# Kernel tuning notes

Measured on AMD Instinct MI355X. Metric: run time of the kernel, lower is better.

Reference implementation:

```python
import jax, jax.numpy as jnp
import numpy as np

H = 2048      # hidden_dim
DI = 4096     # intermediate_size
N = 128       # state_size
NH = 64       # num_heads
P = 64        # head_dim
K = 4         # conv kernel
CH = 256      # chunk size
L = 4096      # seq len
DT_MIN, DT_MAX = 1e-3, 1e2


def setup_inputs() -> dict:
    key = jax.random.key(0)
    ks = jax.random.split(key, 8)
    conv_dim = DI + 2 * N
    x = jax.random.normal(ks[0], (L, H), jnp.float32)
    W_in = jax.random.normal(ks[1], (DI + 2 * N + NH, H), jnp.float32) / np.sqrt(H)
    conv_w = jax.random.normal(ks[2], (conv_dim, 1, K), jnp.float32) / np.sqrt(K)
    conv_b = jax.random.normal(ks[3], (conv_dim,), jnp.float32) * 0.01
    u = jax.random.uniform(ks[4], (NH,))
    dt = jnp.exp(u * (np.log(0.1) - np.log(0.001)) + np.log(0.001))
    dt = jnp.maximum(dt, 1e-4)
    dt_bias = dt + jnp.log(-jnp.expm1(-dt))   # inverse-softplus init
    A_log = jnp.log(jax.random.uniform(ks[5], (NH,), minval=1.0, maxval=16.0))
    D = jnp.ones((NH,), jnp.float32)
    norm_w = jnp.ones((DI,), jnp.float32)
    W_out = jax.random.normal(ks[6], (H, DI), jnp.float32) / np.sqrt(DI)
    return dict(x=x, W_in=W_in, conv_w=conv_w, conv_b=conv_b, dt_bias=dt_bias,
                A_log=A_log, D=D, norm_w=norm_w, W_out=W_out)


def _causal_decay(a):
    # a: [..., T] per-step log-decays -> exp(segment sum) as lower-tri [..., T, T]
    T = a.shape[-1]
    strict = jnp.tril(jnp.ones((T, T), bool), -1)
    full = jnp.tril(jnp.ones((T, T), bool), 0)
    s = jnp.cumsum(jnp.where(strict, a[..., None], 0.0), axis=-2)
    return jnp.where(full, jnp.exp(s), 0.0)


def reference(x, W_in, conv_w, conv_b, dt_bias, A_log, D, norm_w, W_out):
    conv_dim = DI + 2 * N
    xBCdt = x @ W_in.T                                  # [L, DI+2N+NH]
    xBC, dt = xBCdt[:, :conv_dim], xBCdt[:, conv_dim:]
    # causal depthwise conv1d + SiLU
    z = jax.lax.conv_general_dilated(
        xBC.T[None], conv_w, (1,), [(K - 1, 0)],
        dimension_numbers=('NCH', 'OIH', 'NCH'),
        feature_group_count=conv_dim)[0] + conv_b[:, None]
    xBC = jax.nn.silu(z.T)                              # [L, conv_dim]
    x_ssm = xBC[:, :DI].reshape(L, NH, P)
    Bm = xBC[:, DI:DI + N]                              # [L, N] shared over heads
    Cm = xBC[:, DI + N:]                                # [L, N]
    dt = jnp.clip(jax.nn.softplus(dt + dt_bias), DT_MIN, DT_MAX)  # [L, NH]
    A = -jnp.exp(A_log.astype(jnp.float32))             # [NH]
    dA = dt * A                                         # [L, NH]
    xdt = x_ssm * dt[:, :, None]                        # [L, NH, P]
    nc = L // CH
    xc = xdt.reshape(nc, CH, NH, P)
    Bc = Bm.reshape(nc, CH, N)
    Cc = Cm.reshape(nc, CH, N)
    dAc = dA.reshape(nc, CH, NH)
    A_cs = jnp.cumsum(dAc, axis=1)                      # [c, k, h]
    # intra-chunk (diagonal blocks)
    Lmat = _causal_decay(dAc.transpose(0, 2, 1))        # [c, h, k, k]
    Y_diag = jnp.einsum('ckn,csn,chks,cshp->ckhp', Cc, Bc, Lmat, xc)
    # per-chunk right states
    decay_states = jnp.exp(A_cs[:, -1:, :] - A_cs)      # [c, k, h]
    states = jnp.einsum('ckn,ckh,ckhp->chpn', Bc, decay_states, xc)
    # inter-chunk recurrence (no initial state)
    chunk_sum = A_cs[:, -1, :].T                        # [h, c]
    dec = _causal_decay(jnp.pad(chunk_sum, ((0, 0), (1, 0))))  # [h, c+1, c+1]
    states = jnp.concatenate([jnp.zeros((1, NH, P, N), states.dtype), states], 0)
    new_states = jnp.einsum('hzc,chpn->zhpn', dec, states)      # [c+1, h, p, n]
    prev = new_states[:-1]                              # [c, h, p, n]
    Y_off = jnp.einsum('ckn,chpn,ckh->ckhp', Cc, prev, jnp.exp(A_cs))
    Y = (Y_diag + Y_off).reshape(L, NH, P) + x_ssm * D[None, :, None]
    y = Y.reshape(L, DI)
    # RMSNorm
    var = jnp.mean(jnp.square(y.astype(jnp.float32)), -1, keepdims=True)
    y = (y * jax.lax.rsqrt(var + 1e-6)) * norm_w
    return y @ W_out.T
```

## Files before the change

### kernel.cpp

```cpp
#include <hip/hip_runtime.h>


typedef __bf16 bf16;
typedef __bf16 bf16x8 __attribute__((ext_vector_type(8)));
typedef __bf16 bf16x4 __attribute__((ext_vector_type(4)));
typedef float  f32x4  __attribute__((ext_vector_type(4)));

#define DEV static __device__ __forceinline__

DEV f32x4 mfma16(bf16x8 a, bf16x8 b, f32x4 c) {
  return __builtin_amdgcn_mfma_f32_16x16x32_bf16(a, b, c, 0, 0, 0);
}

DEV void gll16(const bf16* g, bf16* l) {
  __builtin_amdgcn_global_load_lds(
      (const __attribute__((address_space(1))) unsigned int*)g,
      (__attribute__((address_space(3))) unsigned int*)l, 16, 0, 0);
}

#define BAR()   asm volatile("s_barrier" ::: "memory")
#define VMW(n)  asm volatile("s_waitcnt vmcnt(" #n ")" ::: "memory")

template <int NT, int LD, bool F32OUT>
__global__ __launch_bounds__(512, 4) void gemm_kernel(
    const bf16* __restrict__ Abase, const bf16* __restrict__ Bbase,
    float* __restrict__ Cf, bf16* __restrict__ Cb0, bf16* __restrict__ Cb1,
    int ldc, int ntN) {
  __shared__ __align__(16) bf16 lds[3 * 12288];
  const int tid = threadIdx.x;
  const int wid = tid >> 6, lane = tid & 63;
  const int lrow = lane & 15;
  const int lc = lane >> 4;
  const int wm = wid & 3, wn = wid >> 2;
  const int bx = blockIdx.x / ntN, by = blockIdx.x % ntN;
  const int row0 = bx * 256, col0 = by * 128;
  const bf16* A = Abase + (size_t)blockIdx.y * (NT * 32);
  const bf16* B = Bbase + (size_t)blockIdx.y * (NT * 32);

  const bf16* gA[2];
  const bf16* gB0;
#pragma unroll
  for (int q = 0; q < 2; ++q) {
    int P = q * 8192 + tid * 16;
    int Lq = P ^ (((P >> 7) & 3) << 4);
    int srow = Lq >> 6;
    int selem = (Lq & 63) >> 1;
    gA[q] = A + (size_t)(row0 + srow) * LD + selem;
  }
  {
    int P = tid * 16;
    int Lq = P ^ (((P >> 7) & 3) << 4);
    int srow = Lq >> 6;
    int selem = (Lq & 63) >> 1;
    gB0 = B + (size_t)(col0 + srow) * LD + selem;
  }
  auto stage = [&](int s, int ko) {
    bf16* sl = lds + s * 12288;
    gll16(gA[0] + ko, sl + tid * 8);
    gll16(gA[1] + ko, sl + 4096 + tid * 8);
    gll16(gB0 + ko, sl + 8192 + tid * 8);
  };
  auto rdA = [&](int s, int m) -> bf16x8 {
    int row = wm * 64 + m * 16 + lrow;
    int off = row * 64 + ((lc ^ ((row >> 1) & 3)) << 4);
    return *(const bf16x8*)((const char*)lds + s * 24576 + off);
  };
  auto rdB = [&](int s, int n) -> bf16x8 {
    int row = wn * 64 + n * 16 + lrow;
    int off = row * 64 + ((lc ^ ((row >> 1) & 3)) << 4);
    return *(const bf16x8*)((const char*)lds + s * 24576 + 16384 + off);
  };

  f32x4 acc[4][4] = {};
  stage(0, 0);
  stage(1, 32);
  int rs = 0, ws = 2;
  for (int t = 0; t < NT; ++t) {
    if (t + 1 < NT) { VMW(3); } else { VMW(0); }
    BAR();
    if (t + 2 < NT) stage(ws, (t + 2) * 32);
    bf16x8 b0 = rdB(rs, 0), b1 = rdB(rs, 1), b2 = rdB(rs, 2), b3 = rdB(rs, 3);
#pragma unroll
    for (int m = 0; m < 4; ++m) {
      bf16x8 a = rdA(rs, m);
      acc[m][0] = mfma16(a, b0, acc[m][0]);
      acc[m][1] = mfma16(a, b1, acc[m][1]);
      acc[m][2] = mfma16(a, b2, acc[m][2]);
      acc[m][3] = mfma16(a, b3, acc[m][3]);
    }
    rs = (rs == 2) ? 0 : rs + 1;
    ws = (ws == 2) ? 0 : ws + 1;
  }
  const int orow = lc * 4;
  if (F32OUT) {
#pragma unroll
    for (int m = 0; m < 4; ++m)
#pragma unroll
      for (int n = 0; n < 4; ++n)
#pragma unroll
        for (int i = 0; i < 4; ++i) {
          int r = row0 + wm * 64 + m * 16 + orow + i;
          int c = col0 + wn * 64 + n * 16 + lrow;
          Cf[(size_t)r * ldc + c] = acc[m][n][i];
        }
  } else {
    bf16* C = blockIdx.y ? Cb1 : Cb0;
#pragma unroll
    for (int m = 0; m < 4; ++m)
#pragma unroll
      for (int n = 0; n < 4; ++n)
#pragma unroll
        for (int i = 0; i < 4; ++i) {
          int r = row0 + wm * 64 + m * 16 + orow + i;
          int c = col0 + wn * 64 + n * 16 + lrow;
          C[(size_t)r * ldc + c] = (bf16)acc[m][n][i];
        }
  }
}

__global__ __launch_bounds__(256) void add2b_kernel(
    const bf16* __restrict__ a, const bf16* __restrict__ b,
    float* __restrict__ o, long n8) {
  long i = (long)blockIdx.x * blockDim.x + threadIdx.x;
  long stride = (long)gridDim.x * blockDim.x;
  for (; i < n8; i += stride) {
    bf16x8 va = ((const bf16x8*)a)[i];
    bf16x8 vb = ((const bf16x8*)b)[i];
    float4 o0, o1;
    o0.x = (float)va[0] + (float)vb[0];
    o0.y = (float)va[1] + (float)vb[1];
    o0.z = (float)va[2] + (float)vb[2];
    o0.w = (float)va[3] + (float)vb[3];
    o1.x = (float)va[4] + (float)vb[4];
    o1.y = (float)va[5] + (float)vb[5];
    o1.z = (float)va[6] + (float)vb[6];
    o1.w = (float)va[7] + (float)vb[7];
    ((float4*)o)[i * 2] = o0;
    ((float4*)o)[i * 2 + 1] = o1;
  }
}

__global__ __launch_bounds__(256) void cast_f2b_kernel(
    const float* __restrict__ in, bf16* __restrict__ out, long n4) {
  long i = (long)blockIdx.x * blockDim.x + threadIdx.x;
  long stride = (long)gridDim.x * blockDim.x;
  for (; i < n4; i += stride) {
    float4 v = ((const float4*)in)[i];
    bf16x4 o = {(bf16)v.x, (bf16)v.y, (bf16)v.z, (bf16)v.w};
    ((bf16x4*)out)[i] = o;
  }
}

__global__ __launch_bounds__(256) void cast_pad_kernel(
    const float* __restrict__ in, bf16* __restrict__ out, long n4, long valid4) {
  long i = (long)blockIdx.x * blockDim.x + threadIdx.x;
  long stride = (long)gridDim.x * blockDim.x;
  for (; i < n4; i += stride) {
    bf16x4 o = {(bf16)0.f, (bf16)0.f, (bf16)0.f, (bf16)0.f};
    if (i < valid4) {
      float4 v = ((const float4*)in)[i];
      o = bf16x4{(bf16)v.x, (bf16)v.y, (bf16)v.z, (bf16)v.w};
    }
    ((bf16x4*)out)[i] = o;
  }
}

__global__ __launch_bounds__(256) void dt_scan_kernel(
    const float* __restrict__ xBCdt, const float* __restrict__ dt_bias,
    const float* __restrict__ A_log, float* __restrict__ dt,
    float* __restrict__ Acs, float* __restrict__ decayO,
    float* __restrict__ expAcs, float* __restrict__ csum) {
  const int c = blockIdx.x, h = blockIdx.y;
  const int k = threadIdx.x;
  const int t = c * 256 + k;
  __shared__ float buf[256];
  float raw = xBCdt[(size_t)t * 4608 + 4352 + h] + dt_bias[h];
  float dtv = raw > 20.f ? raw : log1pf(__expf(raw));
  dtv = fminf(fmaxf(dtv, 0.001f), 100.f);
  dt[(size_t)t * 64 + h] = dtv;
  float dA = -__expf(A_log[h]) * dtv;
  buf[k] = dA;
  __syncthreads();
  for (int off = 1; off < 256; off <<= 1) {
    float add = (k >= off) ? buf[k - off] : 0.f;
    __syncthreads();
    buf[k] += add;
    __syncthreads();
  }
  float v = buf[k];
  float total = buf[255];
  size_t base = (size_t)(c * 64 + h) * 256 + k;
  Acs[base] = v;
  expAcs[base] = __expf(v);
  decayO[base] = __expf(total - v);
  if (k == 0) csum[c * 64 + h] = total;
}

__global__ __launch_bounds__(256) void conv_kernel(
    const float* __restrict__ xBCdt, const float* __restrict__ conv_w,
    const float* __restrict__ conv_b, const float* __restrict__ dt,
    bf16* __restrict__ XS, bf16* __restrict__ XDT_T, bf16* __restrict__ Bm,
    bf16* __restrict__ BT, bf16* __restrict__ Cm) {
  const int t0 = blockIdx.x * 64;
  const int c0 = blockIdx.y * 64;
  __shared__ float lin[67 * 64];
  __shared__ bf16 tr[64 * 72];
  const int tid = threadIdx.x;
  for (int idx = tid; idx < 67 * 64; idx += 256) {
    int r = idx >> 6, cc = idx & 63;
    int gt = t0 + r - 3;
    lin[idx] = (gt >= 0) ? xBCdt[(size_t)gt * 4608 + c0 + cc] : 0.f;
  }
  __syncthreads();
  const int cl = tid & 63, tg = tid >> 6;
  const int ch = c0 + cl;
  const float w0 = conv_w[ch * 4 + 0], w1 = conv_w[ch * 4 + 1];
  const float w2 = conv_w[ch * 4 + 2], w3 = conv_w[ch * 4 + 3];
  const float bb = conv_b[ch];
  float vals[16];
  for (int j = 0; j < 16; ++j) {
    int tl = tg * 16 + j;
    float s = bb + lin[tl * 64 + cl] * w0 + lin[(tl + 1) * 64 + cl] * w1 +
              lin[(tl + 2) * 64 + cl] * w2 + lin[(tl + 3) * 64 + cl] * w3;
    vals[j] = s / (1.f + __expf(-s));
  }
  if (c0 < 4096) {
    const int hh = c0 >> 6;
    for (int j = 0; j < 16; ++j) {
      int t = t0 + tg * 16 + j;
      XS[(size_t)t * 4096 + ch] = (bf16)vals[j];
    }
    __syncthreads();
    for (int j = 0; j < 16; ++j) {
      int tl = tg * 16 + j;
      float dtv = dt[(size_t)(t0 + tl) * 64 + hh];
      tr[cl * 72 + tl] = (bf16)(vals[j] * dtv);
    }
    __syncthreads();
    int p = tid >> 2, toff = (tid & 3) * 16;
    bf16* dst = XDT_T + (size_t)(hh * 64 + p) * 4096 + t0 + toff;
    *(bf16x8*)(dst) = *(const bf16x8*)(tr + p * 72 + toff);
    *(bf16x8*)(dst + 8) = *(const bf16x8*)(tr + p * 72 + toff + 8);
  } else if (c0 < 4224) {
    const int n0 = c0 - 4096;
    for (int j = 0; j < 16; ++j) {
      int t = t0 + tg * 16 + j;
      Bm[(size_t)t * 128 + n0 + cl] = (bf16)vals[j];
    }
    __syncthreads();
    for (int j = 0; j < 16; ++j) tr[cl * 72 + tg * 16 + j] = (bf16)vals[j];
    __syncthreads();
    int p = tid >> 2, toff = (tid & 3) * 16;
    bf16* dst = BT + (size_t)(n0 + p) * 4096 + t0 + toff;
    *(bf16x8*)(dst) = *(const bf16x8*)(tr + p * 72 + toff);
    *(bf16x8*)(dst + 8) = *(const bf16x8*)(tr + p * 72 + toff + 8);
  } else {
    const int n0 = c0 - 4224;
    for (int j = 0; j < 16; ++j) {
      int t = t0 + tg * 16 + j;
      Cm[(size_t)t * 128 + n0 + cl] = (bf16)vals[j];
    }
  }
}

__global__ __launch_bounds__(256) void gmat_kernel(
    const bf16* __restrict__ Cm, const bf16* __restrict__ Bm,
    bf16* __restrict__ G) {
  const int c = blockIdx.x, kt = blockIdx.y, st = blockIdx.z;
  const int tid = threadIdx.x;
  const int wave = tid >> 6, lane = tid & 63;
  const int lrow = lane & 15, lk = (lane >> 4) * 8;
  const int wr = (wave >> 1) * 64, wc = (wave & 1) * 64;
  f32x4 acc[4][4] = {};
  for (int kk = 0; kk < 4; ++kk) {
    bf16x8 aF[4], bF[4];
    for (int m = 0; m < 4; ++m)
      aF[m] = *(const bf16x8*)(Cm + (size_t)(c * 256 + kt * 128 + wr + m * 16 + lrow) * 128 + kk * 32 + lk);
    for (int n = 0; n < 4; ++n)
      bF[n] = *(const bf16x8*)(Bm + (size_t)(c * 256 + st * 128 + wc + n * 16 + lrow) * 128 + kk * 32 + lk);
    for (int m = 0; m < 4; ++m)
      for (int n = 0; n < 4; ++n)
        acc[m][n] = mfma16(aF[m], bF[n], acc[m][n]);
  }
  const int orow = (lane >> 4) * 4;
  for (int m = 0; m < 4; ++m)
    for (int n = 0; n < 4; ++n)
      for (int i = 0; i < 4; ++i) {
        int k = kt * 128 + wr + m * 16 + orow + i;
        int s = st * 128 + wc + n * 16 + lrow;
        G[((size_t)c * 256 + k) * 256 + s] = (bf16)acc[m][n][i];
      }
}

__global__ __launch_bounds__(256) void states_kernel(
    const bf16* __restrict__ XDT_T, const bf16* __restrict__ BT,
    const float* __restrict__ decayO, float* __restrict__ states) {
  const int c = blockIdx.x, h = blockIdx.y;
  __shared__ bf16 Ap[64 * 264];
  __shared__ float sDec[256];
  const int tid = threadIdx.x;
  const int wave = tid >> 6, lane = tid & 63;
  const int lrow = lane & 15, lk = (lane >> 4) * 8;
  sDec[tid] = decayO[(size_t)(c * 64 + h) * 256 + tid];
  __syncthreads();
  {
    int p = tid >> 2, kb = (tid & 3) * 64;
    const bf16* src = XDT_T + (size_t)(h * 64 + p) * 4096 + c * 256 + kb;
    for (int j = 0; j < 8; ++j) {
      bf16x8 v = *(const bf16x8*)(src + j * 8);
      bf16x8 o;
      for (int i = 0; i < 8; ++i) o[i] = (bf16)((float)v[i] * sDec[kb + j * 8 + i]);
      *(bf16x8*)(Ap + p * 264 + kb + j * 8) = o;
    }
  }
  __syncthreads();
  const int nb = wave * 32;
  f32x4 acc[4][2] = {};
  for (int kk = 0; kk < 8; ++kk) {
    bf16x8 aF[4], bF[2];
    for (int m = 0; m < 4; ++m)
      aF[m] = *(const bf16x8*)(Ap + (m * 16 + lrow) * 264 + kk * 32 + lk);
    for (int n = 0; n < 2; ++n)
      bF[n] = *(const bf16x8*)(BT + (size_t)(nb + n * 16 + lrow) * 4096 + c * 256 + kk * 32 + lk);
    for (int m = 0; m < 4; ++m)
      for (int n = 0; n < 2; ++n)
        acc[m][n] = mfma16(aF[m], bF[n], acc[m][n]);
  }
  float* st = states + (size_t)(c * 64 + h) * 64 * 128;
  const int orow = (lane >> 4) * 4;
  for (int m = 0; m < 4; ++m)
    for (int n = 0; n < 2; ++n)
      for (int i = 0; i < 4; ++i)
        st[(size_t)(m * 16 + orow + i) * 128 + nb + n * 16 + lrow] = acc[m][n][i];
}

__global__ __launch_bounds__(128) void chunk_rec_kernel(
    const float* __restrict__ states, const float* __restrict__ csum,
    bf16* __restrict__ prev) {
  const int h = blockIdx.x, p = blockIdx.y;
  const int n = threadIdx.x;
  size_t base = (size_t)h * 64 * 128 + (size_t)p * 128 + n;
  float run = 0.f;
  for (int c = 0; c < 16; ++c) {
    size_t idx = (size_t)c * 64 * 64 * 128 + base;
    prev[idx] = (bf16)run;
    run = run * __expf(csum[c * 64 + h]) + states[idx];
  }
}

__global__ __launch_bounds__(256) void ydiag_kernel(
    const bf16* __restrict__ Cm, const bf16* __restrict__ prev,
    const bf16* __restrict__ Gb, const float* __restrict__ Acs,
    const float* __restrict__ expAcs, const bf16* __restrict__ XDT_T,
    float* __restrict__ Y) {
  const int c = blockIdx.x, h = blockIdx.y;
  __shared__ float sAcs[256];
  __shared__ float sExp[256];
  __shared__ __align__(16) bf16 pv[64 * 136];
  __shared__ __align__(16) bf16 xd[64 * 264];
  const int tid = threadIdx.x;
  const int wave = tid >> 6, lane = tid & 63;
  const int lrow = lane & 15, lk = (lane >> 4) * 8;
  const int wv16 = wave * 16;
  sAcs[tid] = Acs[(size_t)(c * 64 + h) * 256 + tid];
  sExp[tid] = expAcs[(size_t)(c * 64 + h) * 256 + tid];
  {
    int r = tid >> 2, q = (tid & 3) * 32;
    const bf16* src = prev + (size_t)(c * 64 + h) * 8192 + r * 128 + q;
    bf16* dst = pv + r * 136 + q;
    for (int j = 0; j < 4; ++j)
      *(bf16x8*)(dst + j * 8) = *(const bf16x8*)(src + j * 8);
  }
  {
    int r = tid >> 2, q = (tid & 3) * 64;
    const bf16* src = XDT_T + (size_t)(h * 64 + r) * 4096 + c * 256 + q;
    bf16* dst = xd + r * 264 + q;
    for (int j = 0; j < 8; ++j)
      *(bf16x8*)(dst + j * 8) = *(const bf16x8*)(src + j * 8);
  }
  __syncthreads();
  f32x4 acc[4][4] = {};
  bf16x8 aYo[4][4];
#pragma unroll
  for (int kk = 0; kk < 4; ++kk)
#pragma unroll
    for (int m = 0; m < 4; ++m)
      aYo[kk][m] = *(const bf16x8*)(Cm + (size_t)(c * 256 + m * 64 + wv16 + lrow) * 128 + kk * 32 + lk);
#pragma unroll
  for (int kk = 0; kk < 4; ++kk) {
    bf16x8 bF[4];
#pragma unroll
    for (int n = 0; n < 4; ++n)
      bF[n] = *(const bf16x8*)(pv + (n * 16 + lrow) * 136 + kk * 32 + lk);
#pragma unroll
    for (int m = 0; m < 4; ++m)
#pragma unroll
      for (int n = 0; n < 4; ++n)
        acc[m][n] = mfma16(aYo[kk][m], bF[n], acc[m][n]);
  }
  const int orow = (lane >> 4) * 4;
#pragma unroll
  for (int m = 0; m < 4; ++m)
#pragma unroll
    for (int i = 0; i < 4; ++i) {
      float e = sExp[m * 64 + wv16 + orow + i];
      for (int n = 0; n < 4; ++n) acc[m][n][i] *= e;
    }
  const bf16* Gp = Gb + (size_t)c * 65536;
#pragma unroll
  for (int stile = 0; stile < 4; ++stile) {
    const int s0 = stile * 64;
    bf16x8 graw[2][4];
#pragma unroll
    for (int kk = 0; kk < 2; ++kk)
#pragma unroll
      for (int m = 0; m < 4; ++m)
        if (m * 64 + wv16 + 15 >= s0) {
          int row = m * 64 + wv16 + lrow;
          graw[kk][m] = *(const bf16x8*)(Gp + (size_t)row * 256 + s0 + kk * 32 + lk);
        }
    bf16x8 bF[2][4];
#pragma unroll
    for (int kk = 0; kk < 2; ++kk)
#pragma unroll
      for (int n = 0; n < 4; ++n)
        bF[kk][n] = *(const bf16x8*)(xd + (n * 16 + lrow) * 264 + s0 + kk * 32 + lk);
#pragma unroll
    for (int kk = 0; kk < 2; ++kk)
#pragma unroll
      for (int m = 0; m < 4; ++m) {
        if (m * 64 + wv16 + 15 < s0) continue;
        const int row = m * 64 + wv16 + lrow;
        const float ak = sAcs[row];
        bf16x8 af;
#pragma unroll
        for (int j = 0; j < 8; ++j) {
          int s = s0 + kk * 32 + lk + j;
          float v = (float)graw[kk][m][j] * __expf(ak - sAcs[s]);
          if (s > row) v = 0.f;
          af[j] = (bf16)v;
        }
#pragma unroll
        for (int n = 0; n < 4; ++n)
          acc[m][n] = mfma16(af, bF[kk][n], acc[m][n]);
      }
  }
#pragma unroll
  for (int m = 0; m < 4; ++m)
#pragma unroll
    for (int n = 0; n < 4; ++n)
#pragma unroll
      for (int i = 0; i < 4; ++i) {
        int t = c * 256 + m * 64 + wv16 + orow + i;
        int col = h * 64 + n * 16 + lrow;
        Y[(size_t)t * 4096 + col] = acc[m][n][i];
      }
}

__global__ __launch_bounds__(256) void rmsnorm_kernel(
    const float* __restrict__ Y, const bf16* __restrict__ XS,
    const float* __restrict__ Dp, const float* __restrict__ norm_w,
    bf16* __restrict__ out) {
  const int row = blockIdx.x;
  const float4* y4 = (const float4*)(Y + (size_t)row * 4096);
  const bf16x4* xs4 = (const bf16x4*)(XS + (size_t)row * 4096);
  float4 v[4];
  float ss = 0.f;
  for (int j = 0; j < 4; ++j) {
    int c4 = threadIdx.x + j * 256;
    float4 y = y4[c4];
    bf16x4 xs = xs4[c4];
    float d = Dp[(c4 * 4) >> 6];
    y.x += (float)xs[0] * d;
    y.y += (float)xs[1] * d;
    y.z += (float)xs[2] * d;
    y.w += (float)xs[3] * d;
    v[j] = y;
    ss += y.x * y.x + y.y * y.y + y.z * y.z + y.w * y.w;
  }
  for (int off = 32; off; off >>= 1) ss += __shfl_down(ss, off, 64);
  __shared__ float ws[4];
  if ((threadIdx.x & 63) == 0) ws[threadIdx.x >> 6] = ss;
  __syncthreads();
  float scale = rsqrtf((ws[0] + ws[1] + ws[2] + ws[3]) / 4096.f + 1e-6f);
  for (int j = 0; j < 4; ++j) {
    int col = (threadIdx.x + j * 256) * 4;
    float4 w = *(const float4*)(norm_w + col);
    bf16x4 o = {(bf16)(v[j].x * scale * w.x), (bf16)(v[j].y * scale * w.y),
                (bf16)(v[j].z * scale * w.z), (bf16)(v[j].w * scale * w.w)};
    *(bf16x4*)(out + (size_t)row * 4096 + col) = o;
  }
}

extern "C" void kernel_launch(void* const* d_in, const int* in_sizes, int n_in,
                              void* d_out, int out_size, void* d_ws, size_t ws_size,
                              hipStream_t stream) {
  const float* x       = (const float*)d_in[0];
  const float* W_in    = (const float*)d_in[1];
  const float* conv_w  = (const float*)d_in[2];
  const float* conv_b  = (const float*)d_in[3];
  const float* dt_bias = (const float*)d_in[4];
  const float* A_log   = (const float*)d_in[5];
  const float* Dp      = (const float*)d_in[6];
  const float* norm_w  = (const float*)d_in[7];
  const float* W_out   = (const float*)d_in[8];

  size_t o = 0;
  char* base = (char*)d_ws;
  auto take = [&](size_t b) {
    char* p = base + o;
    o += (b + 255) & ~(size_t)255;
    return (void*)p;
  };
  bf16*  xb     = (bf16*)take((size_t)4096 * 2048 * 2);
  bf16*  winb   = (bf16*)take((size_t)4608 * 2048 * 2);
  float* xBCdt  = (float*)take((size_t)4096 * 4608 * 4);
  float* dtg    = (float*)take((size_t)4096 * 64 * 4);
  float* Acs    = (float*)take((size_t)4096 * 64 * 4);
  float* decayO = (float*)take((size_t)4096 * 64 * 4);
  float* expA   = (float*)take((size_t)4096 * 64 * 4);
  float* csum   = (float*)take((size_t)16 * 64 * 4);
  bf16*  XS     = (bf16*)take((size_t)4096 * 4096 * 2);
  bf16*  XDT_T  = (bf16*)take((size_t)4096 * 4096 * 2);
  bf16*  Bm     = (bf16*)take((size_t)4096 * 128 * 2);
  bf16*  BT     = (bf16*)take((size_t)4096 * 128 * 2);
  bf16*  Cm     = (bf16*)take((size_t)4096 * 128 * 2);
  float* Y      = (float*)take((size_t)4096 * 4096 * 4);
  bf16*  Gb     = (bf16*)((char*)xBCdt);
  float* states = (float*)((char*)xBCdt + (size_t)4194304);
  bf16*  prev   = (bf16*)((char*)xBCdt + (size_t)37748736);
  bf16*  woutb  = (bf16*)((char*)xBCdt + (size_t)54525952);
  bf16*  ynorm  = xb;
  bf16*  p2a    = XS;
  bf16*  p2b    = XDT_T;

  cast_f2b_kernel<<<2048, 256, 0, stream>>>(x, xb, (long)4096 * 2048 / 4);
  cast_pad_kernel<<<2048, 256, 0, stream>>>(W_in, winb, (long)4608 * 2048 / 4,
                                            (long)4416 * 2048 / 4);
  gemm_kernel<64, 2048, true><<<dim3(576, 1), 512, 0, stream>>>(
      xb, winb, xBCdt, nullptr, nullptr, 4608, 36);
  dt_scan_kernel<<<dim3(16, 64), 256, 0, stream>>>(xBCdt, dt_bias, A_log, dtg,
                                                   Acs, decayO, expA, csum);
  conv_kernel<<<dim3(64, 68), 256, 0, stream>>>(xBCdt, conv_w, conv_b, dtg, XS,
                                                XDT_T, Bm, BT, Cm);
  gmat_kernel<<<dim3(16, 2, 2), 256, 0, stream>>>(Cm, Bm, Gb);
  states_kernel<<<dim3(16, 64), 256, 0, stream>>>(XDT_T, BT, decayO, states);
  chunk_rec_kernel<<<dim3(64, 64), 128, 0, stream>>>(states, csum, prev);
  cast_f2b_kernel<<<2048, 256, 0, stream>>>(W_out, woutb, (long)2048 * 4096 / 4);
  ydiag_kernel<<<dim3(16, 64), 256, 0, stream>>>(Cm, prev, Gb, Acs, expA,
                                                 XDT_T, Y);
  rmsnorm_kernel<<<4096, 256, 0, stream>>>(Y, XS, Dp, norm_w, ynorm);
  gemm_kernel<64, 4096, false><<<dim3(256, 2), 512, 0, stream>>>(
      ynorm, woutb, nullptr, p2a, p2b, 2048, 16);
  add2b_kernel<<<2048, 256, 0, stream>>>(p2a, p2b, (float*)d_out,
                                         (long)4096 * 2048 / 8);
}
```

Before: 352.4 us.

## Store in-projection and Y in bf16, widen GEMM per-wave tiles, split dt output

The in-projection GEMM now writes its xBC result in bf16 instead of fp32 and writes the dt columns separately as fp32 into a compact buffer. The conv and dt-scan kernels read these narrower buffers. The Y intermediate between ydiag and rmsnorm is also stored in bf16, which halves those memory passes. Separately, the GEMM drops to 256 threads per block, with each wave computing 128x64 instead of 64x64, raising MFMA work per LDS B-fragment read at the cost of more accumulator registers. The bf16 storage adds rounding error to conv inputs and to Y.

New measurement: 337.9 us. 4.1% less time.

```diff
diff --git a/kernel.cpp b/kernel.cpp
--- a/kernel.cpp
+++ b/kernel.cpp
@@ -21,47 +21,49 @@
 #define BAR()   asm volatile("s_barrier" ::: "memory")
 #define VMW(n)  asm volatile("s_waitcnt vmcnt(" #n ")" ::: "memory")
 
-template <int NT, int LD, bool F32OUT>
-__global__ __launch_bounds__(512, 4) void gemm_kernel(
+template <int NT, int LD, bool DTC>
+__global__ __launch_bounds__(256, 2) void gemm_kernel(
     const bf16* __restrict__ Abase, const bf16* __restrict__ Bbase,
-    float* __restrict__ Cf, bf16* __restrict__ Cb0, bf16* __restrict__ Cb1,
+    bf16* __restrict__ C0, bf16* __restrict__ C1, float* __restrict__ dtf,
     int ldc, int ntN) {
   __shared__ __align__(16) bf16 lds[3 * 12288];
   const int tid = threadIdx.x;
   const int wid = tid >> 6, lane = tid & 63;
   const int lrow = lane & 15;
   const int lc = lane >> 4;
-  const int wm = wid & 3, wn = wid >> 2;
+  const int wm = wid & 1, wn = wid >> 1;
   const int bx = blockIdx.x / ntN, by = blockIdx.x % ntN;
   const int row0 = bx * 256, col0 = by * 128;
   const bf16* A = Abase + (size_t)blockIdx.y * (NT * 32);
   const bf16* B = Bbase + (size_t)blockIdx.y * (NT * 32);
 
-  const bf16* gA[2];
-  const bf16* gB0;
-#pragma unroll
-  for (int q = 0; q < 2; ++q) {
-    int P = q * 8192 + tid * 16;
+  const bf16* gA[4];
+  const bf16* gB[2];
+#pragma unroll
+  for (int q = 0; q < 4; ++q) {
+    int P = q * 4096 + tid * 16;
     int Lq = P ^ (((P >> 7) & 3) << 4);
     int srow = Lq >> 6;
     int selem = (Lq & 63) >> 1;
     gA[q] = A + (size_t)(row0 + srow) * LD + selem;
   }
-  {
-    int P = tid * 16;
+#pragma unroll
+  for (int q = 0; q < 2; ++q) {
+    int P = q * 4096 + tid * 16;
     int Lq = P ^ (((P >> 7) & 3) << 4);
     int srow = Lq >> 6;
     int selem = (Lq & 63) >> 1;
-    gB0 = B + (size_t)(col0 + srow) * LD + selem;
+    gB[q] = B + (size_t)(col0 + srow) * LD + selem;
   }
   auto stage = [&](int s, int ko) {
     bf16* sl = lds + s * 12288;
-    gll16(gA[0] + ko, sl + tid * 8);
-    gll16(gA[1] + ko, sl + 4096 + tid * 8);
-    gll16(gB0 + ko, sl + 8192 + tid * 8);
+#pragma unroll
+    for (int q = 0; q < 4; ++q) gll16(gA[q] + ko, sl + q * 2048 + tid * 8);
+#pragma unroll
+    for (int q = 0; q < 2; ++q) gll16(gB[q] + ko, sl + 8192 + q * 2048 + tid * 8);
   };
   auto rdA = [&](int s, int m) -> bf16x8 {
-    int row = wm * 64 + m * 16 + lrow;
+    int row = wm * 128 + m * 16 + lrow;
     int off = row * 64 + ((lc ^ ((row >> 1) & 3)) << 4);
     return *(const bf16x8*)((const char*)lds + s * 24576 + off);
   };
@@ -71,17 +73,17 @@
     return *(const bf16x8*)((const char*)lds + s * 24576 + 16384 + off);
   };
 
-  f32x4 acc[4][4] = {};
+  f32x4 acc[8][4] = {};
   stage(0, 0);
   stage(1, 32);
   int rs = 0, ws = 2;
   for (int t = 0; t < NT; ++t) {
-    if (t + 1 < NT) { VMW(3); } else { VMW(0); }
+    if (t + 1 < NT) { VMW(6); } else { VMW(0); }
     BAR();
     if (t + 2 < NT) stage(ws, (t + 2) * 32);
     bf16x8 b0 = rdB(rs, 0), b1 = rdB(rs, 1), b2 = rdB(rs, 2), b3 = rdB(rs, 3);
 #pragma unroll
-    for (int m = 0; m < 4; ++m) {
+    for (int m = 0; m < 8; ++m) {
       bf16x8 a = rdA(rs, m);
       acc[m][0] = mfma16(a, b0, acc[m][0]);
       acc[m][1] = mfma16(a, b1, acc[m][1]);
@@ -91,29 +93,28 @@
     rs = (rs == 2) ? 0 : rs + 1;
     ws = (ws == 2) ? 0 : ws + 1;
   }
+  bf16* C = blockIdx.y ? C1 : C0;
   const int orow = lc * 4;
-  if (F32OUT) {
-#pragma unroll
-    for (int m = 0; m < 4; ++m)
+#pragma unroll
+  for (int m = 0; m < 8; ++m)
+#pragma unroll
+    for (int n = 0; n < 4; ++n)
+#pragma unroll
+      for (int i = 0; i < 4; ++i) {
+        int r = row0 + wm * 128 + m * 16 + orow + i;
+        int c = col0 + wn * 64 + n * 16 + lrow;
+        C[(size_t)r * ldc + c] = (bf16)acc[m][n][i];
+      }
+  if (DTC && by == 34 && wn == 0) {
+#pragma unroll
+    for (int m = 0; m < 8; ++m)
 #pragma unroll
       for (int n = 0; n < 4; ++n)
 #pragma unroll
         for (int i = 0; i < 4; ++i) {
-          int r = row0 + wm * 64 + m * 16 + orow + i;
-          int c = col0 + wn * 64 + n * 16 + lrow;
-          Cf[(size_t)r * ldc + c] = acc[m][n][i];
-        }
-  } else {
-    bf16* C = blockIdx.y ? Cb1 : Cb0;
-#pragma unroll
-    for (int m = 0; m < 4; ++m)
-#pragma unroll
-      for (int n = 0; n < 4; ++n)
-#pragma unroll
-        for (int i = 0; i < 4; ++i) {
-          int r = row0 + wm * 64 + m * 16 + orow + i;
-          int c = col0 + wn * 64 + n * 16 + lrow;
-          C[(size_t)r * ldc + c] = (bf16)acc[m][n][i];
+          int r = row0 + wm * 128 + m * 16 + orow + i;
+          int h = n * 16 + lrow;
+          dtf[(size_t)r * 64 + h] = acc[m][n][i];
         }
   }
 }
@@ -166,7 +167,7 @@
 }
 
 __global__ __launch_bounds__(256) void dt_scan_kernel(
-    const float* __restrict__ xBCdt, const float* __restrict__ dt_bias,
+    const float* __restrict__ dtf, const float* __restrict__ dt_bias,
     const float* __restrict__ A_log, float* __restrict__ dt,
     float* __restrict__ Acs, float* __restrict__ decayO,
     float* __restrict__ expAcs, float* __restrict__ csum) {
@@ -174,7 +175,7 @@
   const int k = threadIdx.x;
   const int t = c * 256 + k;
   __shared__ float buf[256];
-  float raw = xBCdt[(size_t)t * 4608 + 4352 + h] + dt_bias[h];
+  float raw = dtf[(size_t)t * 64 + h] + dt_bias[h];
   float dtv = raw > 20.f ? raw : log1pf(__expf(raw));
   dtv = fminf(fmaxf(dtv, 0.001f), 100.f);
   dt[(size_t)t * 64 + h] = dtv;
@@ -197,7 +198,7 @@
 }
 
 __global__ __launch_bounds__(256) void conv_kernel(
-    const float* __restrict__ xBCdt, const float* __restrict__ conv_w,
+    const bf16* __restrict__ xbc, const float* __restrict__ conv_w,
     const float* __restrict__ conv_b, const float* __restrict__ dt,
     bf16* __restrict__ XS, bf16* __restrict__ XDT_T, bf16* __restrict__ Bm,
     bf16* __restrict__ BT, bf16* __restrict__ Cm) {
@@ -206,10 +207,18 @@
   __shared__ float lin[67 * 64];
   __shared__ bf16 tr[64 * 72];
   const int tid = threadIdx.x;
-  for (int idx = tid; idx < 67 * 64; idx += 256) {
-    int r = idx >> 6, cc = idx & 63;
+  for (int v = tid; v < 67 * 16; v += 256) {
+    int r = v >> 4, c4 = (v & 15) * 4;
     int gt = t0 + r - 3;
-    lin[idx] = (gt >= 0) ? xBCdt[(size_t)gt * 4608 + c0 + cc] : 0.f;
+    float4 f = {0.f, 0.f, 0.f, 0.f};
+    if (gt >= 0) {
+      bf16x4 b = *(const bf16x4*)(xbc + (size_t)gt * 4608 + c0 + c4);
+      f.x = (float)b[0]; f.y = (float)b[1]; f.z = (float)b[2]; f.w = (float)b[3];
+    }
+    lin[r * 64 + c4 + 0] = f.x;
+    lin[r * 64 + c4 + 1] = f.y;
+    lin[r * 64 + c4 + 2] = f.z;
+    lin[r * 64 + c4 + 3] = f.w;
   }
   __syncthreads();
   const int cl = tid & 63, tg = tid >> 6;
@@ -352,7 +361,7 @@
     const bf16* __restrict__ Cm, const bf16* __restrict__ prev,
     const bf16* __restrict__ Gb, const float* __restrict__ Acs,
     const float* __restrict__ expAcs, const bf16* __restrict__ XDT_T,
-    float* __restrict__ Y) {
+    bf16* __restrict__ Yb) {
   const int c = blockIdx.x, h = blockIdx.y;
   __shared__ float sAcs[256];
   __shared__ float sExp[256];
@@ -453,28 +462,29 @@
       for (int i = 0; i < 4; ++i) {
         int t = c * 256 + m * 64 + wv16 + orow + i;
         int col = h * 64 + n * 16 + lrow;
-        Y[(size_t)t * 4096 + col] = acc[m][n][i];
+        Yb[(size_t)t * 4096 + col] = (bf16)acc[m][n][i];
       }
 }
 
 __global__ __launch_bounds__(256) void rmsnorm_kernel(
-    const float* __restrict__ Y, const bf16* __restrict__ XS,
+    const bf16* __restrict__ Yb, const bf16* __restrict__ XS,
     const float* __restrict__ Dp, const float* __restrict__ norm_w,
     bf16* __restrict__ out) {
   const int row = blockIdx.x;
-  const float4* y4 = (const float4*)(Y + (size_t)row * 4096);
+  const bf16x4* y4 = (const bf16x4*)(Yb + (size_t)row * 4096);
   const bf16x4* xs4 = (const bf16x4*)(XS + (size_t)row * 4096);
   float4 v[4];
   float ss = 0.f;
   for (int j = 0; j < 4; ++j) {
     int c4 = threadIdx.x + j * 256;
-    float4 y = y4[c4];
+    bf16x4 yb = y4[c4];
     bf16x4 xs = xs4[c4];
     float d = Dp[(c4 * 4) >> 6];
-    y.x += (float)xs[0] * d;
-    y.y += (float)xs[1] * d;
-    y.z += (float)xs[2] * d;
-    y.w += (float)xs[3] * d;
+    float4 y;
+    y.x = (float)yb[0] + (float)xs[0] * d;
+    y.y = (float)yb[1] + (float)xs[1] * d;
+    y.z = (float)yb[2] + (float)xs[2] * d;
+    y.w = (float)yb[3] + (float)xs[3] * d;
     v[j] = y;
     ss += y.x * y.x + y.y * y.y + y.z * y.z + y.w * y.w;
   }
@@ -514,7 +524,8 @@
   };
   bf16*  xb     = (bf16*)take((size_t)4096 * 2048 * 2);
   bf16*  winb   = (bf16*)take((size_t)4608 * 2048 * 2);
-  float* xBCdt  = (float*)take((size_t)4096 * 4608 * 4);
+  bf16*  xbc    = (bf16*)take((size_t)4096 * 4608 * 2);
+  float* dtf    = (float*)take((size_t)4096 * 64 * 4);
   float* dtg    = (float*)take((size_t)4096 * 64 * 4);
   float* Acs    = (float*)take((size_t)4096 * 64 * 4);
   float* decayO = (float*)take((size_t)4096 * 64 * 4);
@@ -525,11 +536,11 @@
   bf16*  Bm     = (bf16*)take((size_t)4096 * 128 * 2);
   bf16*  BT     = (bf16*)take((size_t)4096 * 128 * 2);
   bf16*  Cm     = (bf16*)take((size_t)4096 * 128 * 2);
-  float* Y      = (float*)take((size_t)4096 * 4096 * 4);
-  bf16*  Gb     = (bf16*)((char*)xBCdt);
-  float* states = (float*)((char*)xBCdt + (size_t)4194304);
-  bf16*  prev   = (bf16*)((char*)xBCdt + (size_t)37748736);
-  bf16*  woutb  = (bf16*)((char*)xBCdt + (size_t)54525952);
+  bf16*  Yb     = (bf16*)take((size_t)4096 * 4096 * 2);
+  bf16*  prev   = (bf16*)take((size_t)16 * 64 * 64 * 128 * 2);
+  bf16*  woutb  = (bf16*)take((size_t)2048 * 4096 * 2);
+  bf16*  Gb     = (bf16*)((char*)xbc);
+  float* states = (float*)((char*)xbc + (size_t)4194304);
   bf16*  ynorm  = xb;
   bf16*  p2a    = XS;
   bf16*  p2b    = XDT_T;
@@ -537,21 +548,21 @@
   cast_f2b_kernel<<<2048, 256, 0, stream>>>(x, xb, (long)4096 * 2048 / 4);
   cast_pad_kernel<<<2048, 256, 0, stream>>>(W_in, winb, (long)4608 * 2048 / 4,
                                             (long)4416 * 2048 / 4);
-  gemm_kernel<64, 2048, true><<<dim3(576, 1), 512, 0, stream>>>(
-      xb, winb, xBCdt, nullptr, nullptr, 4608, 36);
-  dt_scan_kernel<<<dim3(16, 64), 256, 0, stream>>>(xBCdt, dt_bias, A_log, dtg,
+  gemm_kernel<64, 2048, true><<<dim3(576, 1), 256, 0, stream>>>(
+      xb, winb, xbc, nullptr, dtf, 4608, 36);
+  dt_scan_kernel<<<dim3(16, 64), 256, 0, stream>>>(dtf, dt_bias, A_log, dtg,
                                                    Acs, decayO, expA, csum);
-  conv_kernel<<<dim3(64, 68), 256, 0, stream>>>(xBCdt, conv_w, conv_b, dtg, XS,
+  conv_kernel<<<dim3(64, 68), 256, 0, stream>>>(xbc, conv_w, conv_b, dtg, XS,
                                                 XDT_T, Bm, BT, Cm);
   gmat_kernel<<<dim3(16, 2, 2), 256, 0, stream>>>(Cm, Bm, Gb);
   states_kernel<<<dim3(16, 64), 256, 0, stream>>>(XDT_T, BT, decayO, states);
   chunk_rec_kernel<<<dim3(64, 64), 128, 0, stream>>>(states, csum, prev);
   cast_f2b_kernel<<<2048, 256, 0, stream>>>(W_out, woutb, (long)2048 * 4096 / 4);
   ydiag_kernel<<<dim3(16, 64), 256, 0, stream>>>(Cm, prev, Gb, Acs, expA,
-                                                 XDT_T, Y);
-  rmsnorm_kernel<<<4096, 256, 0, stream>>>(Y, XS, Dp, norm_w, ynorm);
-  gemm_kernel<64, 4096, false><<<dim3(256, 2), 512, 0, stream>>>(
-      ynorm, woutb, nullptr, p2a, p2b, 2048, 16);
+                                                 XDT_T, Yb);
+  rmsnorm_kernel<<<4096, 256, 0, stream>>>(Yb, XS, Dp, norm_w, ynorm);
+  gemm_kernel<64, 4096, false><<<dim3(256, 2), 256, 0, stream>>>(
+      ynorm, woutb, p2a, p2b, nullptr, 2048, 16);
   add2b_kernel<<<2048, 256, 0, stream>>>(p2a, p2b, (float*)d_out,
                                          (long)4096 * 2048 / 8);
 }
```
